# Kernel optimization log

Hardware: AMD Instinct MI355X
Metric: run time of the kernel (lower is better)

The kernel has to match this reference:

```python
import jax, jax.numpy as jnp
import numpy as np

B, T, N, F = 16, 12, 1024, 128
H, DH, C = 8, 16, 64  # heads, d_head (=d_core//H), core_num; note d_in must equal H*DH
EPS = 1e-5


def setup_inputs() -> dict:
    key = jax.random.key(0)
    ks = jax.random.split(key, 12)
    s = lambda fan_in: 1.0 / np.sqrt(fan_in)
    return {
        "input": jax.random.normal(ks[0], (B, T, N, F), jnp.float32),
        # value Linear(d_in,d_in); weights stored [in,out]
        "W_v": jax.random.normal(ks[1], (F, F), jnp.float32) * s(F),
        "b_v": jax.random.normal(ks[2], (F,), jnp.float32) * s(F),
        # core decomposition params
        "adaptive": jax.random.normal(ks[3], (H, DH, N), jnp.float32),
        "cores": jax.random.normal(ks[4], (H, C, DH), jnp.float32),
        # FFN: Linear(2F -> 8F), GELU, Linear(8F -> F)
        "W1": jax.random.normal(ks[5], (2 * F, 8 * F), jnp.float32) * s(2 * F),
        "b1": jax.random.normal(ks[6], (8 * F,), jnp.float32) * s(2 * F),
        "W2": jax.random.normal(ks[7], (8 * F, F), jnp.float32) * s(8 * F),
        "b2": jax.random.normal(ks[8], (F,), jnp.float32) * s(8 * F),
        # BatchNorm2d(d_in) affine params (training-mode batch stats)
        "gamma": jnp.ones((F,), jnp.float32),
        "beta": jnp.zeros((F,), jnp.float32),
    }


def reference(input, W_v, b_v, adaptive, cores, W1, b1, W2, b2, gamma, beta):
    b, t, n, f = input.shape
    h, dh, _ = adaptive.shape
    # value projection, split heads: [b,t,n,f] -> [b,t,h,dh,n]
    v = input @ W_v + b_v
    v = v.reshape(b, t, n, h, dh).transpose(0, 1, 3, 4, 2)
    # core affinity scores [h,c,n]
    aff = jnp.einsum("hcd,hdn->hcn", cores, adaptive) / np.sqrt(dh)
    a_n2c = jax.nn.softmax(aff, axis=-1)  # softmax over nodes
    a_c2n = jax.nn.softmax(aff, axis=-2)  # softmax over cores
    # two-stage aggregation through cores
    v = jnp.einsum("bthfn,hcn->bthfc", v, a_n2c)
    v = jnp.einsum("bthfc,hcn->bthfn", v, a_c2n)
    # merge heads: [b,t,h,dh,n] -> [b,t,f,n] -> [b,t,n,f]
    v = v.reshape(b, t, f, n).swapaxes(-1, -2)
    # FFN on concat([input - v, v]) (dropout off in eval), residual
    x = jnp.concatenate([input - v, v], axis=-1)
    x = jax.nn.gelu(x @ W1 + b1, approximate=False) @ W2 + b2
    out = x + input
    # BatchNorm2d over channel f (batch stats over b,t,n; biased variance)
    mean = out.mean(axis=(0, 1, 2))
    var = out.var(axis=(0, 1, 2))
    return (out - mean) * jax.lax.rsqrt(var + EPS) * gamma + beta
```

## Files before the change

kernel.cpp:

```cpp
#include <hip/hip_runtime.h>
#include <math.h>

#define BB 16
#define TT 12
#define NN 1024
#define FF 128
#define BT 192
#define BTN 196608
#define CNT ((float)BTN)

typedef unsigned short ushort_t;
typedef __attribute__((ext_vector_type(8))) short bf16x8;
typedef __attribute__((ext_vector_type(4))) float f32x4;

__device__ __forceinline__ ushort_t f2bf(float x) {
    union { float f; unsigned u; } c; c.f = x;
    unsigned r = c.u + 0x7fffu + ((c.u >> 16) & 1u);
    return (ushort_t)(r >> 16);
}
__device__ __forceinline__ float bf2f(ushort_t u) {
    union { unsigned u32; float f; } c; c.u32 = ((unsigned)u) << 16; return c.f;
}
__device__ __forceinline__ unsigned pk2(float a, float b) {
    return (unsigned)f2bf(a) | ((unsigned)f2bf(b) << 16);
}
__device__ __forceinline__ float gelu_f(float x) {
    float u = x * x;
    float s = x * fmaf(u, -0.10294428f, -2.30220852f);
    float e = __builtin_amdgcn_exp2f(s);
    return x * __builtin_amdgcn_rcpf(1.0f + e);
}

__device__ __forceinline__ char* swz512(void* base, int row, int byteoff) {
    return (char*)base + row * 512 + (byteoff ^ ((row & 7) << 4));
}
__device__ __forceinline__ char* swz256(void* base, int row, int byteoff) {
    return (char*)base + row * 256 + (byteoff ^ ((row & 7) << 4));
}

__global__ __launch_bounds__(256) void k_aff(const float* __restrict__ cores,
                                             const float* __restrict__ adaptive,
                                             float* __restrict__ aff) {
    int idx = blockIdx.x * 256 + threadIdx.x;
    int n  = idx & 1023;
    int hc = idx >> 10;
    int h  = hc >> 6;
    const float* cp = cores + hc * 16;
    const float* ap = adaptive + h * 16384 + n;
    float s = 0.f;
#pragma unroll
    for (int d = 0; d < 16; ++d) s = fmaf(cp[d], ap[d * 1024], s);
    aff[idx] = s * 0.25f;
}

__global__ __launch_bounds__(256) void k_sm_n(const float* __restrict__ aff,
                                              ushort_t* __restrict__ out) {
    int row = blockIdx.x;
    const float* p = aff + row * 1024;
    int t = threadIdx.x;
    __shared__ float red[8];
    float v0 = p[t], v1 = p[t + 256], v2 = p[t + 512], v3 = p[t + 768];
    float m = fmaxf(fmaxf(v0, v1), fmaxf(v2, v3));
#pragma unroll
    for (int off = 32; off >= 1; off >>= 1) m = fmaxf(m, __shfl_xor(m, off));
    if ((t & 63) == 0) red[t >> 6] = m;
    __syncthreads();
    m = fmaxf(fmaxf(red[0], red[1]), fmaxf(red[2], red[3]));
    v0 = expf(v0 - m); v1 = expf(v1 - m); v2 = expf(v2 - m); v3 = expf(v3 - m);
    float s = v0 + v1 + v2 + v3;
#pragma unroll
    for (int off = 32; off >= 1; off >>= 1) s += __shfl_xor(s, off);
    __syncthreads();
    if ((t & 63) == 0) red[4 + (t >> 6)] = s;
    __syncthreads();
    s = red[4] + red[5] + red[6] + red[7];
    float inv = 1.0f / s;
    out[row * 1024 + t]       = f2bf(v0 * inv);
    out[row * 1024 + t + 256] = f2bf(v1 * inv);
    out[row * 1024 + t + 512] = f2bf(v2 * inv);
    out[row * 1024 + t + 768] = f2bf(v3 * inv);
}

__global__ __launch_bounds__(256) void k_sm_c(const float* __restrict__ aff,
                                              ushort_t* __restrict__ a_c2nT) {
    __shared__ ushort_t tile[256][72];
    int b = blockIdx.x;
    int h = b >> 2, n0 = (b & 3) * 256;
    int t = threadIdx.x;
    const float* p = aff + h * 65536 + n0 + t;
    float m = -1e30f;
#pragma unroll 8
    for (int c = 0; c < 64; ++c) m = fmaxf(m, p[c * 1024]);
    float s = 0.f;
#pragma unroll 8
    for (int c = 0; c < 64; ++c) s += expf(p[c * 1024] - m);
    float inv = 1.0f / s;
#pragma unroll 8
    for (int c = 0; c < 64; ++c) tile[t][c] = f2bf(expf(p[c * 1024] - m) * inv);
    __syncthreads();
    ushort_t* ob = a_c2nT + ((size_t)h * 1024 + n0) * 64;
    for (int i = t; i < 2048; i += 256) {
        int r = i >> 3, cq = i & 7;
        *(bf16x8*)&ob[r * 64 + cq * 8] = *(bf16x8*)&tile[r][cq * 8];
    }
}

__global__ __launch_bounds__(256) void k_wprep_v(const float* __restrict__ Wv,
                                                 ushort_t* __restrict__ WvT) {
    __shared__ float tile[64][65];
    int b = blockIdx.x;
    int r0 = (b >> 1) * 64, c0 = (b & 1) * 64;
    int t = threadIdx.x;
    for (int i = t; i < 4096; i += 256) {
        int r = i >> 6, c = i & 63;
        tile[r][c] = Wv[(size_t)(r0 + r) * 128 + c0 + c];
    }
    __syncthreads();
    for (int i = t; i < 4096; i += 256) {
        int c = i >> 6, r = i & 63;
        WvT[(size_t)(c0 + c) * 128 + r0 + r] = f2bf(tile[r][c]);
    }
}

__global__ __launch_bounds__(256) void k_wpack1(const float* __restrict__ W1,
                                                ushort_t* __restrict__ W1f) {
    int tid = blockIdx.x * 256 + threadIdx.x;
    int lane = tid & 63, jn = (tid >> 6) & 1, kk = (tid >> 7) & 7;
    int w = (tid >> 10) & 3, ch = tid >> 12;
    int lr = lane & 15, lg = lane >> 4;
    int n = ch * 128 + w * 32 + jn * 16 + lr;
    int kb = kk * 32 + lg * 8;
    ushort_t o[8];
#pragma unroll
    for (int e = 0; e < 8; ++e) o[e] = f2bf(W1[(size_t)(kb + e) * 1024 + n]);
    *(bf16x8*)&W1f[(size_t)tid * 8] = *(bf16x8*)o;
}

__global__ __launch_bounds__(256) void k_wpack2(const float* __restrict__ W2,
                                                ushort_t* __restrict__ W2f) {
    int tid = blockIdx.x * 256 + threadIdx.x;
    int lane = tid & 63, jy = (tid >> 6) & 1, kk = (tid >> 7) & 3;
    int w = (tid >> 9) & 3, ch = tid >> 11;
    int lr = lane & 15, lg = lane >> 4;
    int f = w * 32 + jy * 16 + lr;
    int kb = ch * 128 + kk * 32 + lg * 8;
    ushort_t o[8];
#pragma unroll
    for (int e = 0; e < 8; ++e) o[e] = f2bf(W2[(size_t)(kb + e) * 128 + f]);
    *(bf16x8*)&W2f[(size_t)tid * 8] = *(bf16x8*)o;
}

__global__ __launch_bounds__(256) void k_vs1(const float* __restrict__ input,
                                             const ushort_t* __restrict__ WvT,
                                             const float* __restrict__ bv,
                                             const ushort_t* __restrict__ a_n2c,
                                             ushort_t* __restrict__ T1t) {
    __shared__ __align__(16) ushort_t as_lds[128 * 128];
    __shared__ __align__(16) ushort_t vsT[128 * 128];
    int bt = blockIdx.x;
    int t = threadIdx.x, w = t >> 6, lane = t & 63, lr = lane & 15, lg = lane >> 4;

    f32x4 t1acc[2][4];
#pragma unroll
    for (int hl = 0; hl < 2; ++hl)
#pragma unroll
        for (int mi = 0; mi < 4; ++mi) t1acc[hl][mi] = (f32x4){0.f, 0.f, 0.f, 0.f};

    for (int c8 = 0; c8 < 8; ++c8) {
        int n0 = c8 * 128;
        __syncthreads();
        for (int j = 0; j < 16; ++j) {
            int i = j * 256 + t;
            int r = i >> 5, cq = i & 31;
            float4 f = *(const float4*)&input[((size_t)(bt * 1024 + n0 + r)) * 128 + cq * 4];
            union { uint2 d; ushort_t u[4]; } o;
            o.u[0] = f2bf(f.x); o.u[1] = f2bf(f.y); o.u[2] = f2bf(f.z); o.u[3] = f2bf(f.w);
            *(uint2*)swz256(as_lds, r, cq * 8) = o.d;
        }
        __syncthreads();
        f32x4 vacc[2][8];
#pragma unroll
        for (int mi = 0; mi < 2; ++mi)
#pragma unroll
            for (int jn = 0; jn < 8; ++jn) {
                float bb = bv[jn * 16 + lr];
                vacc[mi][jn] = (f32x4){bb, bb, bb, bb};
            }
#pragma unroll
        for (int ks = 0; ks < 4; ++ks) {
            bf16x8 a[2];
#pragma unroll
            for (int mi = 0; mi < 2; ++mi)
                a[mi] = *(const bf16x8*)swz256(as_lds, w * 32 + mi * 16 + lr, ks * 64 + lg * 16);
#pragma unroll
            for (int jn = 0; jn < 8; ++jn) {
                bf16x8 bfr = *(const bf16x8*)&WvT[(size_t)(jn * 16 + lr) * 128 + ks * 32 + lg * 8];
#pragma unroll
                for (int mi = 0; mi < 2; ++mi)
                    vacc[mi][jn] = __builtin_amdgcn_mfma_f32_16x16x32_bf16(a[mi], bfr, vacc[mi][jn], 0, 0, 0);
            }
        }
#pragma unroll
        for (int mi = 0; mi < 2; ++mi)
#pragma unroll
            for (int jn = 0; jn < 8; ++jn) {
                union { uint2 d; ushort_t u[4]; } o;
                o.u[0] = f2bf(vacc[mi][jn][0]); o.u[1] = f2bf(vacc[mi][jn][1]);
                o.u[2] = f2bf(vacc[mi][jn][2]); o.u[3] = f2bf(vacc[mi][jn][3]);
                *(uint2*)swz256(vsT, jn * 16 + lr, w * 64 + mi * 32 + lg * 8) = o.d;
            }
        __syncthreads();
#pragma unroll
        for (int hl = 0; hl < 2; ++hl) {
            int h = w * 2 + hl;
#pragma unroll
            for (int ks = 0; ks < 4; ++ks) {
                bf16x8 bfr = *(const bf16x8*)swz256(vsT, h * 16 + lr, ks * 64 + lg * 16);
#pragma unroll
                for (int mi = 0; mi < 4; ++mi) {
                    bf16x8 a = *(const bf16x8*)&a_n2c[((size_t)(h * 64 + mi * 16 + lr)) * 1024 + n0 + ks * 32 + lg * 8];
                    t1acc[hl][mi] = __builtin_amdgcn_mfma_f32_16x16x32_bf16(a, bfr, t1acc[hl][mi], 0, 0, 0);
                }
            }
        }
    }
#pragma unroll
    for (int hl = 0; hl < 2; ++hl) {
        int h = w * 2 + hl;
#pragma unroll
        for (int mi = 0; mi < 4; ++mi) {
            union { uint2 d; ushort_t u[4]; } o;
            o.u[0] = f2bf(t1acc[hl][mi][0]); o.u[1] = f2bf(t1acc[hl][mi][1]);
            o.u[2] = f2bf(t1acc[hl][mi][2]); o.u[3] = f2bf(t1acc[hl][mi][3]);
            *(uint2*)&T1t[(((size_t)bt * 8 + h) * 16 + lr) * 64 + mi * 16 + lg * 4] = o.d;
        }
    }
}

__global__ __launch_bounds__(256) void k_ffn(
        const float* __restrict__ input,
        const ushort_t* __restrict__ a_c2nT,
        const ushort_t* __restrict__ T1t,
        const ushort_t* __restrict__ W1f,
        const ushort_t* __restrict__ W2f,
        const float* __restrict__ b1,
        const float* __restrict__ b2,
        float* __restrict__ out,
        float* __restrict__ bn_sum,
        float* __restrict__ bn_sq) {
    __shared__ __align__(16) ushort_t x2s[64 * 256];
    __shared__ __align__(16) ushort_t hids[64 * 128];
    int bt = blockIdx.y;
    int n0 = blockIdx.x * 64;
    int t = threadIdx.x;
    int w = t >> 6, lane = t & 63, lr = lane & 15, lg = lane >> 4;
    int R0 = w * 16;
    int rowbase = bt * 1024 + n0;

    {
        const ushort_t* tp = T1t + ((size_t)(bt * 128) + lr) * 64 + lg * 8;
        const ushort_t* ap = a_c2nT + ((size_t)(n0 + R0 + lr)) * 64 + lg * 8;
#pragma unroll
        for (int h = 0; h < 8; ++h) {
            f32x4 vacc = {0.f, 0.f, 0.f, 0.f};
#pragma unroll
            for (int kk = 0; kk < 2; ++kk) {
                bf16x8 af = *(const bf16x8*)(tp + h * 1024 + kk * 32);
                bf16x8 bf = *(const bf16x8*)(ap + (size_t)h * 65536 + kk * 32);
                vacc = __builtin_amdgcn_mfma_f32_16x16x32_bf16(af, bf, vacc, 0, 0, 0);
            }
            uint2 o;
            o.x = pk2(vacc[0], vacc[1]);
            o.y = pk2(vacc[2], vacc[3]);
            *(uint2*)swz512(x2s, R0 + lr, 256 + h * 32 + lg * 8) = o;
        }
    }
#pragma unroll
    for (int j = 0; j < 8; ++j) {
        int row = R0 + j * 2 + (lane >> 5);
        int cq = lane & 31;
        float4 f = *(const float4*)&input[((size_t)rowbase + row) * 128 + cq * 4];
        union { uint2 d; ushort_t u[4]; } vm;
        vm.d = *(uint2*)swz512(x2s, row, 256 + cq * 8);
        uint2 o;
        o.x = pk2(f.x - bf2f(vm.u[0]), f.y - bf2f(vm.u[1]));
        o.y = pk2(f.z - bf2f(vm.u[2]), f.w - bf2f(vm.u[3]));
        *(uint2*)swz512(x2s, row, cq * 8) = o;
    }
    __syncthreads();

    f32x4 yacc[4][2];
#pragma unroll
    for (int mi = 0; mi < 4; ++mi)
#pragma unroll
        for (int jy = 0; jy < 2; ++jy) {
            float bb = b2[w * 32 + jy * 16 + lr];
            yacc[mi][jy] = (f32x4){bb, bb, bb, bb};
        }

    for (int ch = 0; ch < 8; ++ch) {
        bf16x8 b2r[4][2];
        {
            const ushort_t* w2p = W2f + (((size_t)(ch * 4 + w) * 4) * 2) * 512 + lane * 8;
#pragma unroll
            for (int kk = 0; kk < 4; ++kk)
#pragma unroll
                for (int jy = 0; jy < 2; ++jy)
                    b2r[kk][jy] = *(const bf16x8*)(w2p + (kk * 2 + jy) * 512);
        }

        f32x4 hacc[2][4];
#pragma unroll
        for (int jn = 0; jn < 2; ++jn) {
            f32x4 bb = *(const f32x4*)&b1[ch * 128 + w * 32 + jn * 16 + lg * 4];
#pragma unroll
            for (int mi = 0; mi < 4; ++mi) hacc[jn][mi] = bb;
        }
        const ushort_t* w1p = W1f + ((size_t)(ch * 4 + w) * 16) * 512 + lane * 8;
#pragma unroll
        for (int kk = 0; kk < 8; ++kk) {
            bf16x8 xf[4];
#pragma unroll
            for (int mi = 0; mi < 4; ++mi)
                xf[mi] = *(const bf16x8*)swz512(x2s, mi * 16 + lr, kk * 64 + lg * 16);
#pragma unroll
            for (int jn = 0; jn < 2; ++jn) {
                bf16x8 wf = *(const bf16x8*)(w1p + (kk * 2 + jn) * 512);
#pragma unroll
                for (int mi = 0; mi < 4; ++mi)
                    hacc[jn][mi] = __builtin_amdgcn_mfma_f32_16x16x32_bf16(wf, xf[mi], hacc[jn][mi], 0, 0, 0);
            }
        }
        __syncthreads();
#pragma unroll
        for (int jn = 0; jn < 2; ++jn)
#pragma unroll
            for (int mi = 0; mi < 4; ++mi) {
                uint2 o;
                o.x = pk2(gelu_f(hacc[jn][mi][0]), gelu_f(hacc[jn][mi][1]));
                o.y = pk2(gelu_f(hacc[jn][mi][2]), gelu_f(hacc[jn][mi][3]));
                *(uint2*)swz256(hids, mi * 16 + lr, w * 64 + jn * 32 + lg * 8) = o;
            }
        __syncthreads();
#pragma unroll
        for (int kk = 0; kk < 4; ++kk) {
            bf16x8 a4[4];
#pragma unroll
            for (int mi = 0; mi < 4; ++mi)
                a4[mi] = *(const bf16x8*)swz256(hids, mi * 16 + lr, kk * 64 + lg * 16);
#pragma unroll
            for (int jy = 0; jy < 2; ++jy)
#pragma unroll
                for (int mi = 0; mi < 4; ++mi)
                    yacc[mi][jy] = __builtin_amdgcn_mfma_f32_16x16x32_bf16(a4[mi], b2r[kk][jy], yacc[mi][jy], 0, 0, 0);
        }
    }

    float sacc[2] = {0.f, 0.f}, qacc[2] = {0.f, 0.f};
#pragma unroll
    for (int mi = 0; mi < 4; ++mi)
#pragma unroll
        for (int jy = 0; jy < 2; ++jy)
#pragma unroll
            for (int r = 0; r < 4; ++r) {
                int gr = rowbase + mi * 16 + lg * 4 + r;
                int gc = w * 32 + jy * 16 + lr;
                float val = yacc[mi][jy][r] + input[(size_t)gr * 128 + gc];
                out[(size_t)gr * 128 + gc] = val;
                sacc[jy] += val;
                qacc[jy] += val * val;
            }
#pragma unroll
    for (int jy = 0; jy < 2; ++jy) {
        float s = sacc[jy], q = qacc[jy];
        s += __shfl_xor(s, 16); s += __shfl_xor(s, 32);
        q += __shfl_xor(q, 16); q += __shfl_xor(q, 32);
        if (lg == 0) {
            atomicAdd(&bn_sum[w * 32 + jy * 16 + lr], s);
            atomicAdd(&bn_sq[w * 32 + jy * 16 + lr], q);
        }
    }
}

__global__ void k_bnfin(const float* __restrict__ bn_sum, const float* __restrict__ bn_sq,
                        const float* __restrict__ gamma, const float* __restrict__ beta,
                        float* __restrict__ scale, float* __restrict__ shift) {
    int f = threadIdx.x;
    float mean = bn_sum[f] * (1.0f / CNT);
    float var  = bn_sq[f]  * (1.0f / CNT) - mean * mean;
    float sc = gamma[f] * rsqrtf(var + 1e-5f);
    scale[f] = sc;
    shift[f] = beta[f] - mean * sc;
}

__global__ __launch_bounds__(256) void k_bnapply(float* __restrict__ out,
                                                 const float* __restrict__ scale,
                                                 const float* __restrict__ shift) {
    size_t idx = (size_t)blockIdx.x * 256 + threadIdx.x;
    int c = (int)((idx * 4) & 127);
    float4 v = *(float4*)&out[idx * 4];
    float4 sc = *(const float4*)&scale[c];
    float4 sh = *(const float4*)&shift[c];
    v.x = fmaf(v.x, sc.x, sh.x);
    v.y = fmaf(v.y, sc.y, sh.y);
    v.z = fmaf(v.z, sc.z, sh.z);
    v.w = fmaf(v.w, sc.w, sh.w);
    *(float4*)&out[idx * 4] = v;
}

extern "C" void kernel_launch(void* const* d_in, const int* in_sizes, int n_in,
                              void* d_out, int out_size, void* d_ws, size_t ws_size,
                              hipStream_t stream) {
    const float* input    = (const float*)d_in[0];
    const float* Wv       = (const float*)d_in[1];
    const float* bv       = (const float*)d_in[2];
    const float* adaptive = (const float*)d_in[3];
    const float* cores    = (const float*)d_in[4];
    const float* W1       = (const float*)d_in[5];
    const float* b1       = (const float*)d_in[6];
    const float* W2       = (const float*)d_in[7];
    const float* b2       = (const float*)d_in[8];
    const float* gamma    = (const float*)d_in[9];
    const float* beta     = (const float*)d_in[10];
    float* out = (float*)d_out;
    float* ws  = (float*)d_ws;

    float*    aff    = ws;
    ushort_t* a_n2c  = (ushort_t*)(ws + 524288);
    ushort_t* a_c2nT = (ushort_t*)(ws + 786432);
    ushort_t* T1t    = (ushort_t*)(ws + 1048576);
    ushort_t* W1f    = (ushort_t*)(ws + 1835008);
    ushort_t* W2f    = (ushort_t*)(ws + 1966080);
    ushort_t* WvT    = (ushort_t*)(ws + 2031616);
    float* bn_sum    = ws + 2039808;
    float* bn_sq     = bn_sum + 128;
    float* scale     = bn_sum + 256;
    float* shift     = bn_sum + 384;

    k_aff    <<<2048, 256, 0, stream>>>(cores, adaptive, aff);
    k_sm_n   <<<512, 256, 0, stream>>>(aff, a_n2c);
    k_sm_c   <<<32, 256, 0, stream>>>(aff, a_c2nT);
    k_wprep_v<<<4, 256, 0, stream>>>(Wv, WvT);
    k_wpack1 <<<128, 256, 0, stream>>>(W1, W1f);
    k_wpack2 <<<64, 256, 0, stream>>>(W2, W2f);
    k_vs1    <<<BT, 256, 0, stream>>>(input, WvT, bv, a_n2c, T1t);
    hipMemsetAsync(bn_sum, 0, 256 * sizeof(float), stream);
    k_ffn    <<<dim3(16, BT), 256, 0, stream>>>(input, a_c2nT, T1t, W1f, W2f,
                                                b1, b2, out, bn_sum, bn_sq);
    k_bnfin  <<<1, 128, 0, stream>>>(bn_sum, bn_sq, gamma, beta, scale, shift);
    k_bnapply<<<(out_size / 4) / 256, 256, 0, stream>>>(out, scale, shift);
}
```

Baseline: 445.9 us.

## Split node reduction in value-aggregation kernel across blocks and widen core-softmax grid

The first aggregation kernel now runs a 4-way split over the node dimension (grid BT x 4). Each part writes fp32 partial sums to workspace, and a new reduction kernel adds the four parts and converts to bf16. With only 192 blocks before, the MI355X compute units were underused, so this quadruples the block count. The core-softmax kernel also moves from 32 to 128 blocks, with four threads cooperating per node through shuffles, and keeps its values in registers instead of recomputing exp three times. The cost is an extra kernel launch and about 25 MB of extra fp32 traffic for the partial sums.

```diff
diff --git a/kernel.cpp b/kernel.cpp
--- a/kernel.cpp
+++ b/kernel.cpp
@@ -8,6 +8,7 @@
 #define BT 192
 #define BTN 196608
 #define CNT ((float)BTN)
+#define T1SZ 1572864
 
 typedef unsigned short ushort_t;
 typedef __attribute__((ext_vector_type(8))) short bf16x8;
@@ -83,23 +84,32 @@
 
 __global__ __launch_bounds__(256) void k_sm_c(const float* __restrict__ aff,
                                               ushort_t* __restrict__ a_c2nT) {
-    __shared__ ushort_t tile[256][72];
+    __shared__ ushort_t tile[64][72];
     int b = blockIdx.x;
-    int h = b >> 2, n0 = (b & 3) * 256;
+    int h = b >> 4, n0 = (b & 15) * 64;
     int t = threadIdx.x;
-    const float* p = aff + h * 65536 + n0 + t;
+    int nl = t >> 2, q = t & 3;
+    const float* p = aff + h * 65536 + n0 + nl;
+    float v[16];
     float m = -1e30f;
-#pragma unroll 8
-    for (int c = 0; c < 64; ++c) m = fmaxf(m, p[c * 1024]);
+#pragma unroll
+    for (int i = 0; i < 16; ++i) {
+        v[i] = p[(q * 16 + i) * 1024];
+        m = fmaxf(m, v[i]);
+    }
+    m = fmaxf(m, __shfl_xor(m, 1));
+    m = fmaxf(m, __shfl_xor(m, 2));
     float s = 0.f;
-#pragma unroll 8
-    for (int c = 0; c < 64; ++c) s += expf(p[c * 1024] - m);
+#pragma unroll
+    for (int i = 0; i < 16; ++i) { v[i] = expf(v[i] - m); s += v[i]; }
+    s += __shfl_xor(s, 1);
+    s += __shfl_xor(s, 2);
     float inv = 1.0f / s;
-#pragma unroll 8
-    for (int c = 0; c < 64; ++c) tile[t][c] = f2bf(expf(p[c * 1024] - m) * inv);
+#pragma unroll
+    for (int i = 0; i < 16; ++i) tile[nl][q * 16 + i] = f2bf(v[i] * inv);
     __syncthreads();
     ushort_t* ob = a_c2nT + ((size_t)h * 1024 + n0) * 64;
-    for (int i = t; i < 2048; i += 256) {
+    for (int i = t; i < 512; i += 256) {
         int r = i >> 3, cq = i & 7;
         *(bf16x8*)&ob[r * 64 + cq * 8] = *(bf16x8*)&tile[r][cq * 8];
     }
@@ -154,10 +164,11 @@
                                              const ushort_t* __restrict__ WvT,
                                              const float* __restrict__ bv,
                                              const ushort_t* __restrict__ a_n2c,
-                                             ushort_t* __restrict__ T1t) {
+                                             float* __restrict__ T1p) {
     __shared__ __align__(16) ushort_t as_lds[128 * 128];
     __shared__ __align__(16) ushort_t vsT[128 * 128];
     int bt = blockIdx.x;
+    int part = blockIdx.y;
     int t = threadIdx.x, w = t >> 6, lane = t & 63, lr = lane & 15, lg = lane >> 4;
 
     f32x4 t1acc[2][4];
@@ -166,7 +177,7 @@
 #pragma unroll
         for (int mi = 0; mi < 4; ++mi) t1acc[hl][mi] = (f32x4){0.f, 0.f, 0.f, 0.f};
 
-    for (int c8 = 0; c8 < 8; ++c8) {
+    for (int c8 = part * 2; c8 < part * 2 + 2; ++c8) {
         int n0 = c8 * 128;
         __syncthreads();
         for (int j = 0; j < 16; ++j) {
@@ -224,17 +235,29 @@
             }
         }
     }
+    float* op = T1p + (size_t)part * T1SZ;
 #pragma unroll
     for (int hl = 0; hl < 2; ++hl) {
         int h = w * 2 + hl;
 #pragma unroll
-        for (int mi = 0; mi < 4; ++mi) {
-            union { uint2 d; ushort_t u[4]; } o;
-            o.u[0] = f2bf(t1acc[hl][mi][0]); o.u[1] = f2bf(t1acc[hl][mi][1]);
-            o.u[2] = f2bf(t1acc[hl][mi][2]); o.u[3] = f2bf(t1acc[hl][mi][3]);
-            *(uint2*)&T1t[(((size_t)bt * 8 + h) * 16 + lr) * 64 + mi * 16 + lg * 4] = o.d;
-        }
-    }
+        for (int mi = 0; mi < 4; ++mi)
+            *(f32x4*)&op[(((size_t)bt * 8 + h) * 16 + lr) * 64 + mi * 16 + lg * 4] = t1acc[hl][mi];
+    }
+}
+
+__global__ __launch_bounds__(256) void k_t1conv(const float* __restrict__ T1p,
+                                                ushort_t* __restrict__ T1t) {
+    size_t i4 = ((size_t)blockIdx.x * 256 + threadIdx.x) * 4;
+    float4 s = *(const float4*)&T1p[i4];
+#pragma unroll
+    for (int p = 1; p < 4; ++p) {
+        float4 v = *(const float4*)&T1p[(size_t)p * T1SZ + i4];
+        s.x += v.x; s.y += v.y; s.z += v.z; s.w += v.w;
+    }
+    uint2 o;
+    o.x = pk2(s.x, s.y);
+    o.y = pk2(s.z, s.w);
+    *(uint2*)&T1t[i4] = o;
 }
 
 __global__ __launch_bounds__(256) void k_ffn(
@@ -436,14 +459,16 @@
     float* bn_sq     = bn_sum + 128;
     float* scale     = bn_sum + 256;
     float* shift     = bn_sum + 384;
+    float* T1p       = ws + 2097152;
 
     k_aff    <<<2048, 256, 0, stream>>>(cores, adaptive, aff);
     k_sm_n   <<<512, 256, 0, stream>>>(aff, a_n2c);
-    k_sm_c   <<<32, 256, 0, stream>>>(aff, a_c2nT);
+    k_sm_c   <<<128, 256, 0, stream>>>(aff, a_c2nT);
     k_wprep_v<<<4, 256, 0, stream>>>(Wv, WvT);
     k_wpack1 <<<128, 256, 0, stream>>>(W1, W1f);
     k_wpack2 <<<64, 256, 0, stream>>>(W2, W2f);
-    k_vs1    <<<BT, 256, 0, stream>>>(input, WvT, bv, a_n2c, T1t);
+    k_vs1    <<<dim3(BT, 4), 256, 0, stream>>>(input, WvT, bv, a_n2c, T1p);
+    k_t1conv <<<1536, 256, 0, stream>>>(T1p, T1t);
     hipMemsetAsync(bn_sum, 0, 256 * sizeof(float), stream);
     k_ffn    <<<dim3(16, BT), 256, 0, stream>>>(input, a_c2nT, T1t, W1f, W2f,
                                                 b1, b2, out, bn_sum, bn_sq);
```

After: 425.0 us. -4.7%, faster.
